# Kernel tuning notes

Hardware: AMD Instinct MI355X
Metric: run time of the kernel (lower is better)

## Reference

```python
import jax, jax.numpy as jnp
import numpy as np

REPLACE_PROB = 0.1  # from init_kwargs


def _build_logits(p):
    """3x3x3 table: logits3[prev1, prev2, k] = log P(x_t=k | x_{t-1}=prev1, x_{t-2}=prev2).
    Matches torch: cond2d[m[t-2]][m[t-1]] == Categorical(tmp[m[t-1]][m[t-2]]),
    with the special renormalized row tmp[2][1] = [0, s/(p+s), p/(p+s)]."""
    s = 1.0 - 2.0 * p
    tmp = np.tile(np.array([p, s, p], dtype=np.float32), (3, 3, 1))
    tmp[2, 1] = np.array([0.0, s / (p + s), p / (p + s)], dtype=np.float32)
    return jnp.log(jnp.asarray(tmp))  # log(0) -> -inf disallows that outcome


def _gen_mindex(key, n_batch, T, logits3):
    """Generate (B, T) gather indices. Positions 0,1 and T-1 fixed to state 1;
    positions 2..T-2 sampled from the 2nd-order Markov chain. Then shift by
    arange(T)-1 to turn states {0,1,2} into source indices {t-1, t, t+1}."""
    n_steps = T - 3
    keys = jax.random.split(key, n_steps)

    def step(carry, k):
        prev2, prev1 = carry  # each (B,) int32
        lg = logits3[prev1, prev2]  # (B, 3)
        s = jax.random.categorical(k, lg).astype(jnp.int32)  # (B,)
        return (prev1, s), s

    init = (jnp.ones(n_batch, jnp.int32), jnp.ones(n_batch, jnp.int32))
    _, samp = jax.lax.scan(step, init, keys)  # (T-3, B)
    mid = samp.T  # (B, T-3)
    ones2 = jnp.ones((n_batch, 2), jnp.int32)
    ones1 = jnp.ones((n_batch, 1), jnp.int32)
    mindex = jnp.concatenate([ones2, mid, ones1], axis=1)  # (B, T)
    return mindex + (jnp.arange(T, dtype=jnp.int32) - 1)


def setup_inputs() -> dict:
    key = jax.random.key(0)
    B, I, T = 16, 256, 8192
    x = jax.random.normal(key, (B, I, T), dtype=jnp.float32)
    return {"x": x, "seed": 0}


def reference(x, seed):
    B, I, T = x.shape
    logits3 = _build_logits(REPLACE_PROB)
    mindex = _gen_mindex(jax.random.key(seed), B, T, logits3)  # (B, T)
    # per-batch gather along time: y[b, :, t] = x[b, :, mindex[b, t]]
    y = jnp.take_along_axis(x, mindex[:, None, :], axis=2)  # (B, I, T)
    return y[:, :, 1:-1]  # (B, I, T-2)
```

## Files before the change

### kernel.cpp

```cpp
#include <hip/hip_runtime.h>
#include <math.h>
#include <stdint.h>

#define T_LEN 8192
#define NSTEP 8189
#define NB 16
#define NI 256
#define OUTT 8190
#define CHUNK 128
#define NCHUNK 64

__device__ __forceinline__ uint32_t rotl32(uint32_t v, int r) {
  return (v << r) | (v >> (32 - r));
}

__device__ __forceinline__ void tf2x32(uint32_t k0, uint32_t k1,
                                       uint32_t x0, uint32_t x1,
                                       uint32_t& o0, uint32_t& o1) {
  uint32_t k2 = k0 ^ k1 ^ 0x1BD11BDAu;
  x0 += k0; x1 += k1;
  x0 += x1; x1 = rotl32(x1, 13); x1 ^= x0;
  x0 += x1; x1 = rotl32(x1, 15); x1 ^= x0;
  x0 += x1; x1 = rotl32(x1, 26); x1 ^= x0;
  x0 += x1; x1 = rotl32(x1,  6); x1 ^= x0;
  x0 += k1; x1 += k2 + 1u;
  x0 += x1; x1 = rotl32(x1, 17); x1 ^= x0;
  x0 += x1; x1 = rotl32(x1, 29); x1 ^= x0;
  x0 += x1; x1 = rotl32(x1, 16); x1 ^= x0;
  x0 += x1; x1 = rotl32(x1, 24); x1 ^= x0;
  x0 += k2; x1 += k0 + 2u;
  x0 += x1; x1 = rotl32(x1, 13); x1 ^= x0;
  x0 += x1; x1 = rotl32(x1, 15); x1 ^= x0;
  x0 += x1; x1 = rotl32(x1, 26); x1 ^= x0;
  x0 += x1; x1 = rotl32(x1,  6); x1 ^= x0;
  x0 += k0; x1 += k1 + 3u;
  x0 += x1; x1 = rotl32(x1, 17); x1 ^= x0;
  x0 += x1; x1 = rotl32(x1, 29); x1 ^= x0;
  x0 += x1; x1 = rotl32(x1, 16); x1 ^= x0;
  x0 += x1; x1 = rotl32(x1, 24); x1 ^= x0;
  x0 += k1; x1 += k2 + 4u;
  x0 += x1; x1 = rotl32(x1, 13); x1 ^= x0;
  x0 += x1; x1 = rotl32(x1, 15); x1 ^= x0;
  x0 += x1; x1 = rotl32(x1, 26); x1 ^= x0;
  x0 += x1; x1 = rotl32(x1,  6); x1 ^= x0;
  x0 += k2; x1 += k0 + 5u;
  o0 = x0; o1 = x1;
}

__device__ __forceinline__ float f32log_cr(float x) {
  return (float)log((double)x);
}

__device__ __forceinline__ float bits_to_gumbel(uint32_t bits) {
  uint32_t fb = (bits >> 9) | 0x3F800000u;
  float u = __uint_as_float(fb) - 1.0f;
  if (u == 0.0f) u = 1.17549435e-38f;
  float inner = f32log_cr(u);
  float outer = f32log_cr(-inner);
  return -outer;
}

__device__ __forceinline__ int chain_step(int sigma, uint32_t dv) {
  int s = (sigma == 5) ? (int)(dv >> 2) : (int)(dv & 3u);
  return (sigma % 3) * 3 + s;
}

__global__ void k_dec_spec(const int* __restrict__ seedp,
                           uint8_t* __restrict__ dec,
                           uint8_t* __restrict__ Mend) {
  __shared__ uint8_t ld[CHUNK];
  int c = blockIdx.x, b = blockIdx.y;
  int t = c * CHUNK + threadIdx.x;

  if (t < NSTEP) {
    uint32_t sk0 = 0u;
    uint32_t sk1 = (uint32_t)seedp[0];
    uint32_t kt0, kt1;
    tf2x32(sk0, sk1, 0u, (uint32_t)t, kt0, kt1);

    float g[3];
#pragma unroll
    for (int e = 0; e < 3; ++e) {
      uint32_t o0, o1;
      tf2x32(kt0, kt1, 0u, (uint32_t)(3 * b + e), o0, o1);
      g[e] = bits_to_gumbel(o0 ^ o1);
    }

    const double pd = 0.1;
    const double sd = 1.0 - 2.0 * 0.1;
    const float Lp  = f32log_cr((float)pd);
    const float Ls  = f32log_cr((float)sd);
    const float Lb1 = f32log_cr((float)(sd / (pd + sd)));
    const float Lb2 = f32log_cr((float)(pd / (pd + sd)));

    float z0 = g[0] + Lp, z1 = g[1] + Ls, z2 = g[2] + Lp;
    int an = 0; float best = z0;
    if (z1 > best) { best = z1; an = 1; }
    if (z2 > best) { an = 2; }
    int as_ = ((g[2] + Lb2) > (g[1] + Lb1)) ? 2 : 1;

    uint8_t v = (uint8_t)(an | (as_ << 2));
    ld[threadIdx.x] = v;
    dec[b * T_LEN + t] = v;
  }
  __syncthreads();

  if (threadIdx.x < 9) {
    int sigma = threadIdx.x;
    int n = min(CHUNK, NSTEP - c * CHUNK);
    for (int k = 0; k < n; ++k) sigma = chain_step(sigma, ld[k]);
    Mend[(b * NCHUNK + c) * 9 + threadIdx.x] = (uint8_t)sigma;
  }
}

__global__ void k_chain(const uint8_t* __restrict__ dec,
                        const uint8_t* __restrict__ Mend,
                        uint8_t* __restrict__ st2) {
  __shared__ uint8_t m[NCHUNK * 9];
  __shared__ uint8_t entry[NCHUNK];
  int b = blockIdx.x;
  for (int idx = threadIdx.x; idx < NCHUNK * 9; idx += blockDim.x)
    m[idx] = Mend[b * NCHUNK * 9 + idx];
  __syncthreads();
  if (threadIdx.x == 0) {
    int sigma = 4;
    for (int cc = 0; cc < NCHUNK; ++cc) {
      entry[cc] = (uint8_t)sigma;
      sigma = m[cc * 9 + sigma];
    }
  }
  __syncthreads();
  int c = threadIdx.x;
  int t0 = c * CHUNK;
  int sigma = entry[c];
  const uint32_t* dw = (const uint32_t*)(dec + b * T_LEN + t0);
  uint8_t* s2 = st2 + b * T_LEN;
  if (c == 0) s2[0] = 1;
#pragma unroll 8
  for (int wi = 0; wi < CHUNK / 4; ++wi) {
    uint32_t word = dw[wi];
#pragma unroll
    for (int r = 0; r < 4; ++r) {
      int t = t0 + 4 * wi + r;
      uint32_t dv = (word >> (8 * r)) & 0xFFu;
      int s = (sigma == 5) ? (int)(dv >> 2) : (int)(dv & 3u);
      if (t < NSTEP) s2[t + 1] = (uint8_t)s;
      sigma = (sigma % 3) * 3 + s;
    }
  }
}

__global__ void k_gather(const float* __restrict__ x,
                         const uint8_t* __restrict__ st2,
                         float* __restrict__ out) {
  int jt = blockIdx.x * blockDim.x + threadIdx.x;
  int i = blockIdx.y, b = blockIdx.z;
  int j0 = jt * 16;
  size_t row = (size_t)(b * NI + i);
  const float* xr = x + row * (size_t)T_LEN;
  float* orow = out + row * (size_t)OUTT;

  uint4 q = *(const uint4*)(st2 + b * T_LEN + j0);
  uint32_t wbits[4] = {q.x, q.y, q.z, q.w};

  float w[18];
  float4 a0 = *(const float4*)(xr + j0);
  float4 a1 = *(const float4*)(xr + j0 + 4);
  float4 a2 = *(const float4*)(xr + j0 + 8);
  float4 a3 = *(const float4*)(xr + j0 + 12);
  w[0]=a0.x; w[1]=a0.y; w[2]=a0.z; w[3]=a0.w;
  w[4]=a1.x; w[5]=a1.y; w[6]=a1.z; w[7]=a1.w;
  w[8]=a2.x; w[9]=a2.y; w[10]=a2.z; w[11]=a2.w;
  w[12]=a3.x; w[13]=a3.y; w[14]=a3.z; w[15]=a3.w;

  if (j0 + 16 <= OUTT) {
    float2 e = *(const float2*)(xr + j0 + 16);
    w[16] = e.x; w[17] = e.y;
    float res[16];
#pragma unroll
    for (int m = 0; m < 4; ++m) {
      uint32_t ww = wbits[m];
#pragma unroll
      for (int r = 0; r < 4; ++r) {
        int k = 4 * m + r;
        int s = (int)((ww >> (8 * r)) & 0xFFu);
        res[k] = (s == 0) ? w[k] : ((s == 1) ? w[k + 1] : w[k + 2]);
      }
    }
#pragma unroll
    for (int m = 0; m < 8; ++m)
      *(float2*)(orow + j0 + 2 * m) = make_float2(res[2 * m], res[2 * m + 1]);
  } else {
    float res[14];
#pragma unroll
    for (int m = 0; m < 4; ++m) {
      uint32_t ww = wbits[m];
#pragma unroll
      for (int r = 0; r < 4; ++r) {
        int k = 4 * m + r;
        if (k >= 14) break;
        int s = (int)((ww >> (8 * r)) & 0xFFu);
        res[k] = (s == 0) ? w[k] : ((s == 1) ? w[k + 1] : w[k + 2]);
      }
    }
#pragma unroll
    for (int m = 0; m < 7; ++m)
      *(float2*)(orow + j0 + 2 * m) = make_float2(res[2 * m], res[2 * m + 1]);
  }
}

extern "C" void kernel_launch(void* const* d_in, const int* in_sizes, int n_in,
                              void* d_out, int out_size, void* d_ws, size_t ws_size,
                              hipStream_t stream) {
  const float* x   = (const float*)d_in[0];
  const int* seedp = (const int*)d_in[1];
  float* out       = (float*)d_out;

  uint8_t* ws    = (uint8_t*)d_ws;
  uint8_t* dec   = ws;
  uint8_t* st2   = dec + NB * T_LEN;
  uint8_t* Mend  = st2 + NB * T_LEN;

  k_dec_spec<<<dim3(NCHUNK, NB), CHUNK, 0, stream>>>(seedp, dec, Mend);
  k_chain<<<NB, NCHUNK, 0, stream>>>(dec, Mend, st2);
  k_gather<<<dim3(2, NI, NB), 256, 0, stream>>>(x, st2, out);
}
```

Measured before the change: 262.3 us.

## Align gather output stores to 16 bytes per row parity with nontemporal writes

The output row length is 8190, so odd rows start on an 8-byte but not 16-byte boundary. The gather kernel now shifts each thread's 4-element output window by 0 or 2 elements depending on row parity, so every store is an aligned float4. Each element is the first thread's 4 outputs and is written with nontemporal stores. One leftover thread per row handles the 2-element tail, which sits at the end for even rows and the start for odd rows. The grid grows to four times as many threads, each with less work, which raises parallelism but also means more redundant index loads.

```diff
diff --git a/kernel.cpp b/kernel.cpp
--- a/kernel.cpp
+++ b/kernel.cpp
@@ -9,6 +9,9 @@
 #define OUTT 8190
 #define CHUNK 128
 #define NCHUNK 64
+
+typedef float f32x4 __attribute__((ext_vector_type(4)));
+typedef float f32x2 __attribute__((ext_vector_type(2)));
 
 __device__ __forceinline__ uint32_t rotl32(uint32_t v, int r) {
   return (v << r) | (v >> (32 - r));
@@ -153,59 +156,62 @@
 __global__ void k_gather(const float* __restrict__ x,
                          const uint8_t* __restrict__ st2,
                          float* __restrict__ out) {
-  int jt = blockIdx.x * blockDim.x + threadIdx.x;
   int i = blockIdx.y, b = blockIdx.z;
-  int j0 = jt * 16;
-  size_t row = (size_t)(b * NI + i);
-  const float* xr = x + row * (size_t)T_LEN;
-  float* orow = out + row * (size_t)OUTT;
-
-  uint4 q = *(const uint4*)(st2 + b * T_LEN + j0);
-  uint32_t wbits[4] = {q.x, q.y, q.z, q.w};
-
-  float w[18];
-  float4 a0 = *(const float4*)(xr + j0);
-  float4 a1 = *(const float4*)(xr + j0 + 4);
-  float4 a2 = *(const float4*)(xr + j0 + 8);
-  float4 a3 = *(const float4*)(xr + j0 + 12);
-  w[0]=a0.x; w[1]=a0.y; w[2]=a0.z; w[3]=a0.w;
-  w[4]=a1.x; w[5]=a1.y; w[6]=a1.z; w[7]=a1.w;
-  w[8]=a2.x; w[9]=a2.y; w[10]=a2.z; w[11]=a2.w;
-  w[12]=a3.x; w[13]=a3.y; w[14]=a3.z; w[15]=a3.w;
-
-  if (j0 + 16 <= OUTT) {
-    float2 e = *(const float2*)(xr + j0 + 16);
-    w[16] = e.x; w[17] = e.y;
-    float res[16];
-#pragma unroll
-    for (int m = 0; m < 4; ++m) {
-      uint32_t ww = wbits[m];
-#pragma unroll
-      for (int r = 0; r < 4; ++r) {
-        int k = 4 * m + r;
-        int s = (int)((ww >> (8 * r)) & 0xFFu);
-        res[k] = (s == 0) ? w[k] : ((s == 1) ? w[k + 1] : w[k + 2]);
+  int row = b * NI + i;
+  int sig = (row & 1) ? 2 : 0;
+  int k = blockIdx.x * blockDim.x + threadIdx.x;
+  const float* xr = x + (size_t)row * (size_t)T_LEN;
+  float* orow = out + (size_t)row * (size_t)OUTT;
+  const uint8_t* sp = st2 + b * T_LEN;
+
+  if (k < 2047) {
+    int J = 4 * k;
+    float4 A  = *(const float4*)(xr + J);
+    float4 Bv = *(const float4*)(xr + J + 4);
+    uint32_t s0 = *(const uint32_t*)(sp + J);
+    uint32_t s1 = *(const uint32_t*)(sp + J + 4);
+    float w[8] = {A.x, A.y, A.z, A.w, Bv.x, Bv.y, Bv.z, Bv.w};
+
+    float res[4];
+    if (sig == 0) {
+      uint32_t sb[4] = { s0 & 0xFFu, (s0 >> 8) & 0xFFu,
+                         (s0 >> 16) & 0xFFu, s0 >> 24 };
+#pragma unroll
+      for (int m = 0; m < 4; ++m) {
+        uint32_t s = sb[m];
+        res[m] = (s == 0) ? w[m] : ((s == 1) ? w[m + 1] : w[m + 2]);
       }
-    }
-#pragma unroll
-    for (int m = 0; m < 8; ++m)
-      *(float2*)(orow + j0 + 2 * m) = make_float2(res[2 * m], res[2 * m + 1]);
+    } else {
+      uint32_t sb[4] = { (s0 >> 16) & 0xFFu, s0 >> 24,
+                         s1 & 0xFFu, (s1 >> 8) & 0xFFu };
+#pragma unroll
+      for (int m = 0; m < 4; ++m) {
+        uint32_t s = sb[m];
+        res[m] = (s == 0) ? w[m + 2] : ((s == 1) ? w[m + 3] : w[m + 4]);
+      }
+    }
+    f32x4 r = { res[0], res[1], res[2], res[3] };
+    __builtin_nontemporal_store(r, (f32x4*)(orow + J + sig));
   } else {
-    float res[14];
-#pragma unroll
-    for (int m = 0; m < 4; ++m) {
-      uint32_t ww = wbits[m];
-#pragma unroll
-      for (int r = 0; r < 4; ++r) {
-        int k = 4 * m + r;
-        if (k >= 14) break;
-        int s = (int)((ww >> (8 * r)) & 0xFFu);
-        res[k] = (s == 0) ? w[k] : ((s == 1) ? w[k + 1] : w[k + 2]);
-      }
-    }
-#pragma unroll
-    for (int m = 0; m < 7; ++m)
-      *(float2*)(orow + j0 + 2 * m) = make_float2(res[2 * m], res[2 * m + 1]);
+    if (sig == 0) {
+      float4 A = *(const float4*)(xr + 8188);
+      uint32_t s0 = *(const uint32_t*)(sp + 8188);
+      uint32_t b0 = s0 & 0xFFu, b1 = (s0 >> 8) & 0xFFu;
+      float w0 = A.x, w1 = A.y, w2 = A.z, w3 = A.w;
+      float r0 = (b0 == 0) ? w0 : ((b0 == 1) ? w1 : w2);
+      float r1 = (b1 == 0) ? w1 : ((b1 == 1) ? w2 : w3);
+      f32x2 r = { r0, r1 };
+      __builtin_nontemporal_store(r, (f32x2*)(orow + 8188));
+    } else {
+      float4 A = *(const float4*)(xr);
+      uint32_t s0 = *(const uint32_t*)(sp);
+      uint32_t b0 = s0 & 0xFFu, b1 = (s0 >> 8) & 0xFFu;
+      float w0 = A.x, w1 = A.y, w2 = A.z, w3 = A.w;
+      float r0 = (b0 == 0) ? w0 : ((b0 == 1) ? w1 : w2);
+      float r1 = (b1 == 0) ? w1 : ((b1 == 1) ? w2 : w3);
+      f32x2 r = { r0, r1 };
+      __builtin_nontemporal_store(r, (f32x2*)(orow));
+    }
   }
 }
 
@@ -223,5 +229,5 @@
 
   k_dec_spec<<<dim3(NCHUNK, NB), CHUNK, 0, stream>>>(seedp, dec, Mend);
   k_chain<<<NB, NCHUNK, 0, stream>>>(dec, Mend, st2);
-  k_gather<<<dim3(2, NI, NB), 256, 0, stream>>>(x, st2, out);
-}
+  k_gather<<<dim3(8, NI, NB), 256, 0, stream>>>(x, st2, out);
+}
```

Measured after the change: 251.3 us. -4.2%, faster.
